# Kernel optimization log

Hardware: AMD Instinct MI355X
Metric: run time of the kernel (lower is better)

Reference implementation:

```python
import jax, jax.numpy as jnp
import numpy as np

EPSILON = 0.01        # temperature
DIST_THRESH = 0.2
NUM_ITERS = 8         # sparse_rebalance_iters (== num_iters here)
TOPK = 64             # topk_support
NEG_INF = -1e9


def setup_inputs() -> dict:
    key = jax.random.key(0)
    k1, k2, k3 = jax.random.split(key, 3)
    B, N, M, D = 4, 4096, 4096, 128
    return {
        "source_feats": jax.random.normal(k1, (B, N, D), dtype=jnp.float32),
        "source_locs": jax.random.uniform(k2, (B, N, 2), dtype=jnp.float32),
        "target_locs": jax.random.uniform(k3, (B, M, 2), dtype=jnp.float32),
        "source_valid_mask": jnp.ones((B, N), dtype=bool),
        "target_valid_mask": jnp.ones((B, M), dtype=bool),
    }


def _sinkhorn_attn(source_locs, target_locs, source_valid_mask, target_valid_mask):
    # pairwise squared distances: [B, M, N]
    diff = target_locs[:, :, None, :] - source_locs[:, None, :, :]
    dist_sq = jnp.sum(diff * diff, axis=-1)
    log_k = -dist_sq / (EPSILON + 1e-8)
    valid = (dist_sq < DIST_THRESH ** 2)
    valid = valid & source_valid_mask[:, None, :] & target_valid_mask[:, :, None]

    B, M, N = valid.shape
    topk = min(TOPK, N)
    if topk < N:
        masked_log_k = jnp.where(valid, log_k, NEG_INF)
        _, topk_idx = jax.lax.top_k(masked_log_k, topk)  # [B, M, topk]
        support = jnp.zeros_like(valid).at[
            jnp.arange(B)[:, None, None], jnp.arange(M)[None, :, None], topk_idx
        ].set(True)
        valid = valid & support

    log_k = jnp.where(valid, log_k, NEG_INF)

    v = jnp.zeros((B, 1, N), dtype=log_k.dtype)
    u = jnp.zeros((B, M, 1), dtype=log_k.dtype)
    for _ in range(NUM_ITERS):
        u = -jax.nn.logsumexp(log_k + v, axis=2, keepdims=True)
        v = -jax.nn.logsumexp(log_k + u, axis=1, keepdims=True)
        v = jnp.where(source_valid_mask[:, None, :], v, 0.0)

    attn = jnp.exp(log_k + u + v)              # [B, M, N]
    has_source = valid.any(axis=-1, keepdims=True)  # [B, M, 1]
    return attn, has_source


def reference(source_feats, source_locs, target_locs, source_valid_mask, target_valid_mask):
    attn, has_source = _sinkhorn_attn(source_locs, target_locs,
                                      source_valid_mask, target_valid_mask)
    target_feats = jnp.einsum('bmn,bnd->bmd', attn, source_feats)
    target_feats = target_feats * target_valid_mask[:, :, None].astype(target_feats.dtype)
    target_feats = target_feats * has_source.astype(target_feats.dtype)
    return target_feats
```

## Files before the change

### kernel.cpp

```cpp
#include <hip/hip_runtime.h>
#include <math.h>

#define B 4
#define N 4096
#define M 4096
#define D 128
#define K 64
#define BT 256
#define WPB 4
#define RPW 2
#define CAP 768
#define CUTCAP 128
#define PC 128
#define EPS_DENOM 0.01000001f
#define THRESH2 0.04f
#define GC 16
#define NBCOL (B * N / 16)
#define NBPREP (B * N / 256)

__global__ __launch_bounds__(1024) void k_sort(const float* __restrict__ slocs,
        float4* __restrict__ sPack, int* __restrict__ cellStart,
        int* __restrict__ colcnt, int* __restrict__ E, int* __restrict__ R,
        float* __restrict__ extraF, float* __restrict__ cs){
    __shared__ int hist[256], startS[256], fill[256], wtot[4];
    __shared__ float2 loc[N];
    __shared__ unsigned short scell[N];
    const int b = blockIdx.x, tid = threadIdx.x;
    const int lane = tid & 63, w = tid >> 6;
    const float2* slp = (const float2*)(slocs + (size_t)b * N * 2);

    for (int i = tid; i < N; i += 1024){
        colcnt[b * N + i] = 0;
        cs[b * N + i] = 1.0f;
    }
    if (b == 0){
        if (tid < B){ E[tid] = 0; R[tid] = 0; }
        if (tid < B * D) extraF[tid] = 0.f;
    }

    if (tid < 256){ hist[tid] = 0; fill[tid] = 0; }
    __syncthreads();
    for (int i = tid; i < N; i += 1024){
        float2 p = slp[i];
        int cx = min(GC - 1, max(0, (int)(p.x * (float)GC)));
        int cy = min(GC - 1, max(0, (int)(p.y * (float)GC)));
        int cell = cy * GC + cx;
        loc[i] = p; scell[i] = (unsigned short)cell;
        atomicAdd(&hist[cell], 1);
    }
    __syncthreads();
    int hv = (tid < 256) ? hist[tid] : 0;
    int pre = hv;
    #pragma unroll
    for (int o = 1; o < 64; o <<= 1){ int t2 = __shfl_up(pre, o, 64); if (lane >= o) pre += t2; }
    if (tid < 256 && lane == 63) wtot[w] = pre;
    __syncthreads();
    if (tid < 256){
        int off = 0;
        for (int i = 0; i < w; ++i) off += wtot[i];
        int st = off + pre - hv;
        startS[tid] = st;
        cellStart[b * 257 + tid] = st;
    }
    if (tid == 0) cellStart[b * 257 + 256] = N;
    __syncthreads();
    for (int i = tid; i < N; i += 1024){
        int cell = scell[i];
        int pos = startS[cell] + atomicAdd(&fill[cell], 1);
        float2 p = loc[i];
        sPack[(size_t)b * N + pos] = make_float4(p.x, p.y, __int_as_float(i), 0.f);
    }
}

__global__ __launch_bounds__(BT, 4) void k_build(const float4* __restrict__ sPack,
        const int* __restrict__ cellStart, const float* __restrict__ tlocs,
        float2* __restrict__ csr, int* __restrict__ cnt,
        int* __restrict__ colcnt, float2* __restrict__ csc,
        int* __restrict__ R, float* __restrict__ eu){
    __shared__ int cs[257];
    __shared__ float cd2[WPB][CAP];
    __shared__ int   cn [WPB][CAP];
    __shared__ int   hist[WPB][64];
    __shared__ float cutd[WPB][CUTCAP];
    __shared__ int   cutn[WPB][CUTCAP];
    __shared__ float seld2[WPB][K];
    __shared__ int   seln [WPB][K];

    const int bid  = blockIdx.x;
    const int b    = bid / (M / (WPB * RPW));
    const int m00  = (bid % (M / (WPB * RPW))) * (WPB * RPW);
    const int tid  = threadIdx.x;
    const int w    = tid >> 6;
    const int lane = tid & 63;
    const unsigned long long pmask = (lane == 0) ? 0ull : ((1ull << lane) - 1);
    const float4* sp = sPack + (size_t)b * N;

    for (int i = tid; i < 257; i += BT) cs[i] = cellStart[b * 257 + i];
    __syncthreads();

    for (int r = 0; r < RPW; ++r){
        const int m     = m00 + w * RPW + r;
        const int rowid = b * M + m;

        hist[w][lane] = 0;

        const float tx = tlocs[((size_t)b * M + m) * 2 + 0];
        const float ty = tlocs[((size_t)b * M + m) * 2 + 1];
        const int cy0 = max(0, (int)floorf((ty - 0.2f) * (float)GC - 0.001f));
        const int cy1 = min(GC - 1, (int)floorf((ty + 0.2f) * (float)GC + 0.001f));

        int c = 0;
        for (int cy = cy0; cy <= cy1; ++cy){
            float rowLo = cy * 0.0625f, rowHi = rowLo + 0.0625f;
            float dymin = fmaxf(0.f, fmaxf(rowLo - ty, ty - rowHi));
            float dxm = sqrtf(fmaxf(THRESH2 - dymin * dymin + 1e-5f, 0.f));
            int cx0 = max(0, (int)floorf((tx - dxm) * (float)GC - 0.001f));
            int cx1 = min(GC - 1, (int)floorf((tx + dxm) * (float)GC + 0.001f));
            int s = cs[cy * GC + cx0], e = cs[cy * GC + cx1 + 1];
            for (int j0 = s; j0 < e; j0 += 128){
                int ja = j0 + lane;
                int jb = ja + 64;
                float4 qa = sp[ja];
                float4 qb = sp[jb];
                float dxa = __fsub_rn(tx, qa.x), dya = __fsub_rn(ty, qa.y);
                float d2a = __fadd_rn(__fmul_rn(dxa, dxa), __fmul_rn(dya, dya));
                bool ina = (ja < e) && (d2a < THRESH2);
                unsigned long long mla = __ballot(ina);
                if (ina){
                    int p = c + __popcll(mla & pmask);
                    if (p < CAP){ cd2[w][p] = d2a; cn[w][p] = __float_as_int(qa.z); }
                    atomicAdd(&hist[w][min((int)(d2a * 1600.0f), 63)], 1);
                }
                c += __popcll(mla);
                float dxb = __fsub_rn(tx, qb.x), dyb = __fsub_rn(ty, qb.y);
                float d2b = __fadd_rn(__fmul_rn(dxb, dxb), __fmul_rn(dyb, dyb));
                bool inb = (jb < e) && (d2b < THRESH2);
                unsigned long long mlb = __ballot(inb);
                if (inb){
                    int p = c + __popcll(mlb & pmask);
                    if (p < CAP){ cd2[w][p] = d2b; cn[w][p] = __float_as_int(qb.z); }
                    atomicAdd(&hist[w][min((int)(d2b * 1600.0f), 63)], 1);
                }
                c += __popcll(mlb);
            }
        }
        const int ctot = min(c, CAP);

        int h = hist[w][lane];
        int pre = h;
        #pragma unroll
        for (int o = 1; o < 64; o <<= 1){
            int t2 = __shfl_up(pre, o, 64);
            if (lane >= o) pre += t2;
        }
        int cutB = 64, q = 0;
        if (c > K){
            unsigned long long ge = __ballot(pre >= K);
            int fb = __ffsll((long long)ge) - 1;
            cutB = fb;
            q = K - __shfl(pre - h, fb, 64);
        }

        int base = 0, cutc = 0;
        for (int i0 = 0; i0 < ctot; i0 += 64){
            int i = i0 + lane;
            bool valid = i < ctot;
            float d2 = 1e9f; int n = 0;
            if (valid){ d2 = cd2[w][i]; n = cn[w][i]; }
            int bk = valid ? min((int)(d2 * 1600.0f), 63) : 64;
            bool low = valid && (bk < cutB);
            unsigned long long ml = __ballot(low);
            if (low){
                int p = base + __popcll(ml & pmask);
                seld2[w][p] = d2; seln[w][p] = n;
            }
            base += __popcll(ml);
            if (cutB < 64){
                bool eq = valid && (bk == cutB);
                unsigned long long me = __ballot(eq);
                if (eq){
                    int p = cutc + __popcll(me & pmask);
                    if (p < CUTCAP){ cutd[w][p] = d2; cutn[w][p] = n; }
                }
                cutc += __popcll(me);
            }
        }

        if (c > K){
            int cc = min(cutc, CUTCAP);
            for (int i0 = 0; i0 < CUTCAP; i0 += 64){
                int i = i0 + lane;
                bool sel = false; float d2i = 0.f; int ni = 0;
                if (i < cc){
                    d2i = cutd[w][i]; ni = cutn[w][i];
                    int rank = 0;
                    for (int j = 0; j < cc; ++j){
                        float dj = cutd[w][j]; int nj = cutn[w][j];
                        rank += (dj < d2i) || (dj == d2i && nj < ni);
                    }
                    sel = rank < q;
                }
                unsigned long long ms = __ballot(sel);
                if (sel){
                    int p = base + __popcll(ms & pmask);
                    seld2[w][p] = d2i; seln[w][p] = ni;
                }
                base += __popcll(ms);
                if (i0 + 64 >= cc) break;
            }
        }

        float e = 0.f;
        if (lane < base){
            float d2 = seld2[w][lane];
            int n = seln[w][lane];
            e = expf(-(d2 / EPS_DENOM));
            float2 pr; pr.x = e; pr.y = __int_as_float(n);
            csr[(size_t)rowid * K + lane] = pr;
            int bn = b * N + n;
            int slot = atomicAdd(&colcnt[bn], 1);
            if (slot < PC){
                float2 pc; pc.x = e; pc.y = __int_as_float(rowid);
                csc[(size_t)bn * PC + slot] = pc;
            }
        }
        float rs = e;
        #pragma unroll
        for (int o = 32; o; o >>= 1) rs += __shfl_xor(rs, o, 64);
        if (lane == 0){
            cnt[rowid] = base;
            if (base == 0) atomicAdd(&R[b], 1);
            eu[rowid] = (base == 0) ? 0.f : 1.0f / rs;
        }
    }
}

__global__ __launch_bounds__(256) void kA(const float2* __restrict__ csr,
        const int* __restrict__ cnt, const float* __restrict__ cs,
        const int* __restrict__ E, float* __restrict__ eu){
    int t = blockIdx.x * blockDim.x + threadIdx.x;
    int W = t >> 6, lane = t & 63;
    for (int rr = 0; rr < 4; ++rr){
        int rid = W * 4 + rr;
        int b = rid >> 12;
        int c = cnt[rid];
        float s = 0.f;
        if (lane < c){
            float2 q = csr[(size_t)rid * K + lane];
            s = q.x / cs[(b << 12) + __float_as_int(q.y)];
        }
        #pragma unroll
        for (int o = 32; o; o >>= 1) s += __shfl_xor(s, o, 64);
        int Eb = E[b];
        if (c == 0 && Eb == 0){
            if (lane == 0) eu[rid] = 0.f;
        } else {
            if (Eb > 0) s += (float)Eb;
            if (lane == 0) eu[rid] = 1.0f / s;
        }
    }
}

__global__ __launch_bounds__(256) void kB(const float2* __restrict__ csc,
        const int* __restrict__ colcnt, const float* __restrict__ eu,
        const int* __restrict__ R, float* __restrict__ cs,
        const float* __restrict__ feats, float* __restrict__ extraF, int* __restrict__ E){
    if (blockIdx.x >= NBCOL){
        int t = (blockIdx.x - NBCOL) * 256 + threadIdx.x;
        int lane = t & 63, b = t >> 12;
        int cc = colcnt[t];
        unsigned long long em = __ballot(cc == 0);
        if (lane == 0 && em) atomicAdd(&E[b], __popcll(em));
        if (cc == 0){
            for (int d = 0; d < D; ++d)
                atomicAdd(&extraF[b * D + d], feats[(size_t)t * D + d]);
        }
        return;
    }
    int t = blockIdx.x * blockDim.x + threadIdx.x;
    int W = t >> 6, lane = t & 63;
    for (int rr = 0; rr < 4; ++rr){
        int cid = W * 4 + rr;
        int b = cid >> 12;
        int cc = min(colcnt[cid], PC);
        float s = 0.f;
        for (int p = lane; p < cc; p += 64){
            float2 q = csc[(size_t)cid * PC + p];
            s += q.x * eu[__float_as_int(q.y)];
        }
        #pragma unroll
        for (int o = 32; o; o >>= 1) s += __shfl_xor(s, o, 64);
        if (lane == 0)
            cs[cid] = s + (float)R[b];
    }
}

__global__ __launch_bounds__(256) void k_out(const float* __restrict__ feats,
        const float2* __restrict__ csr, const int* __restrict__ cnt,
        const float* __restrict__ eu, const float* __restrict__ cs,
        const float* __restrict__ extraF, float* __restrict__ out){
    int t = blockIdx.x * blockDim.x + threadIdx.x;
    int rid = t >> 6, lane = t & 63;
    int b = rid >> 12;
    int c = cnt[rid];
    float a = 0.f; int ix = (b << 12);
    if (lane < c){
        float2 q = csr[(size_t)rid * K + lane];
        ix = (b << 12) + __float_as_int(q.y);
        a = q.x * eu[rid] / cs[ix];
    }
    float2 acc = make_float2(0.f, 0.f);
    if (c > 0)
        acc = ((const float2*)extraF)[b * 64 + lane];
    const float2* fb = (const float2*)feats;
    #pragma unroll 4
    for (int k = 0; k < c; ++k){
        float ak = __shfl(a, k, 64);
        int  nk = __shfl(ix, k, 64);
        float2 f = fb[(size_t)nk * 64 + lane];
        acc.x = fmaf(ak, f.x, acc.x);
        acc.y = fmaf(ak, f.y, acc.y);
    }
    ((float2*)out)[(size_t)rid * 64 + lane] = acc;
}

extern "C" void kernel_launch(void* const* d_in, const int* in_sizes, int n_in,
                              void* d_out, int out_size, void* d_ws, size_t ws_size,
                              hipStream_t stream){
    const float* feats = (const float*)d_in[0];
    const float* slocs = (const float*)d_in[1];
    const float* tlocs = (const float*)d_in[2];
    float* out = (float*)d_out;

    char* w = (char*)d_ws;
    size_t off = 0;
    auto carve = [&](size_t bytes) -> void* {
        void* p = w + off;
        off += (bytes + 255) & ~(size_t)255;
        return p;
    };
    float2* csr    = (float2*)carve((size_t)B * M * K * 8);
    float2* csc    = (float2*)carve((size_t)B * N * PC * 8);
    int*   cnt     = (int*)  carve((size_t)B * M * 4);
    int*   colcnt  = (int*)  carve((size_t)B * N * 4);
    float* eu      = (float*)carve((size_t)B * M * 4);
    float* cs      = (float*)carve((size_t)B * N * 4);
    int*   E       = (int*)  carve(B * 4);
    int*   R       = (int*)  carve(B * 4);
    float* extraF  = (float*)carve((size_t)B * D * 4);
    float4* sPack  = (float4*)carve(((size_t)B * N + 128) * 16);
    int*   cellStart = (int*)carve((size_t)B * 257 * 4);

    k_sort<<<B, 1024, 0, stream>>>(slocs, sPack, cellStart, colcnt, E, R, extraF, cs);
    k_build<<<B * M / (WPB * RPW), BT, 0, stream>>>(sPack, cellStart, tlocs,
            csr, cnt, colcnt, csc, R, eu);
    kB<<<NBCOL + NBPREP, 256, 0, stream>>>(csc, colcnt, eu, R, cs, feats, extraF, E);
    for (int it = 2; it <= 8; ++it){
        kA<<<B * M / 16, 256, 0, stream>>>(csr, cnt, cs, E, eu);
        kB<<<NBCOL, 256, 0, stream>>>(csc, colcnt, eu, R, cs, feats, extraF, E);
    }
    k_out<<<B * M / 4, 256, 0, stream>>>(feats, csr, cnt, eu, cs, extraF, out);
}
```

Baseline: 272.9 us.

## Replace candidate buffering with three-pass recompute top-k and separate CSC build kernel

The row-selection kernel stops staging every in-radius candidate in large shared arrays. Instead it makes three passes over the grid cells: build a histogram, gather the cut bucket with per-lane counts, then write the selected entries straight to CSR at prefix-sum offsets. The CSC transpose moves into its own kernel that reads the CSR entries, and rows per wave go from 2 to 4. Less shared memory should allow more occupancy and removes the CAP overflow limit, at the cost of recomputing distances three times and an extra kernel launch with global atomics.

```diff
diff --git a/kernel.cpp b/kernel.cpp
--- a/kernel.cpp
+++ b/kernel.cpp
@@ -8,8 +8,7 @@
 #define K 64
 #define BT 256
 #define WPB 4
-#define RPW 2
-#define CAP 768
+#define RPW 4
 #define CUTCAP 128
 #define PC 128
 #define EPS_DENOM 0.01000001f
@@ -72,19 +71,15 @@
     }
 }
 
-__global__ __launch_bounds__(BT, 4) void k_build(const float4* __restrict__ sPack,
+__global__ __launch_bounds__(BT, 4) void k_sel(const float4* __restrict__ sPack,
         const int* __restrict__ cellStart, const float* __restrict__ tlocs,
         float2* __restrict__ csr, int* __restrict__ cnt,
-        int* __restrict__ colcnt, float2* __restrict__ csc,
         int* __restrict__ R, float* __restrict__ eu){
     __shared__ int cs[257];
-    __shared__ float cd2[WPB][CAP];
-    __shared__ int   cn [WPB][CAP];
-    __shared__ int   hist[WPB][64];
+    __shared__ int hist[WPB][64];
     __shared__ float cutd[WPB][CUTCAP];
     __shared__ int   cutn[WPB][CUTCAP];
-    __shared__ float seld2[WPB][K];
-    __shared__ int   seln [WPB][K];
+    __shared__ int   cutcS[WPB];
 
     const int bid  = blockIdx.x;
     const int b    = bid / (M / (WPB * RPW));
@@ -92,7 +87,6 @@
     const int tid  = threadIdx.x;
     const int w    = tid >> 6;
     const int lane = tid & 63;
-    const unsigned long long pmask = (lane == 0) ? 0ull : ((1ull << lane) - 1);
     const float4* sp = sPack + (size_t)b * N;
 
     for (int i = tid; i < 257; i += BT) cs[i] = cellStart[b * 257 + i];
@@ -103,13 +97,13 @@
         const int rowid = b * M + m;
 
         hist[w][lane] = 0;
+        if (lane == 0) cutcS[w] = 0;
 
         const float tx = tlocs[((size_t)b * M + m) * 2 + 0];
         const float ty = tlocs[((size_t)b * M + m) * 2 + 1];
         const int cy0 = max(0, (int)floorf((ty - 0.2f) * (float)GC - 0.001f));
         const int cy1 = min(GC - 1, (int)floorf((ty + 0.2f) * (float)GC + 0.001f));
 
-        int c = 0;
         for (int cy = cy0; cy <= cy1; ++cy){
             float rowLo = cy * 0.0625f, rowHi = rowLo + 0.0625f;
             float dymin = fmaxf(0.f, fmaxf(rowLo - ty, ty - rowHi));
@@ -118,33 +112,19 @@
             int cx1 = min(GC - 1, (int)floorf((tx + dxm) * (float)GC + 0.001f));
             int s = cs[cy * GC + cx0], e = cs[cy * GC + cx1 + 1];
             for (int j0 = s; j0 < e; j0 += 128){
-                int ja = j0 + lane;
-                int jb = ja + 64;
+                int ja = j0 + lane, jb = ja + 64;
                 float4 qa = sp[ja];
                 float4 qb = sp[jb];
                 float dxa = __fsub_rn(tx, qa.x), dya = __fsub_rn(ty, qa.y);
                 float d2a = __fadd_rn(__fmul_rn(dxa, dxa), __fmul_rn(dya, dya));
-                bool ina = (ja < e) && (d2a < THRESH2);
-                unsigned long long mla = __ballot(ina);
-                if (ina){
-                    int p = c + __popcll(mla & pmask);
-                    if (p < CAP){ cd2[w][p] = d2a; cn[w][p] = __float_as_int(qa.z); }
+                if ((ja < e) && (d2a < THRESH2))
                     atomicAdd(&hist[w][min((int)(d2a * 1600.0f), 63)], 1);
-                }
-                c += __popcll(mla);
                 float dxb = __fsub_rn(tx, qb.x), dyb = __fsub_rn(ty, qb.y);
                 float d2b = __fadd_rn(__fmul_rn(dxb, dxb), __fmul_rn(dyb, dyb));
-                bool inb = (jb < e) && (d2b < THRESH2);
-                unsigned long long mlb = __ballot(inb);
-                if (inb){
-                    int p = c + __popcll(mlb & pmask);
-                    if (p < CAP){ cd2[w][p] = d2b; cn[w][p] = __float_as_int(qb.z); }
+                if ((jb < e) && (d2b < THRESH2))
                     atomicAdd(&hist[w][min((int)(d2b * 1600.0f), 63)], 1);
-                }
-                c += __popcll(mlb);
             }
         }
-        const int ctot = min(c, CAP);
 
         int h = hist[w][lane];
         int pre = h;
@@ -153,85 +133,137 @@
             int t2 = __shfl_up(pre, o, 64);
             if (lane >= o) pre += t2;
         }
-        int cutB = 64, q = 0;
+        const int c = __shfl(pre, 63, 64);
+        int cutB = 64, q = 0, lowTot = min(c, K);
         if (c > K){
             unsigned long long ge = __ballot(pre >= K);
             int fb = __ffsll((long long)ge) - 1;
             cutB = fb;
-            q = K - __shfl(pre - h, fb, 64);
-        }
-
-        int base = 0, cutc = 0;
-        for (int i0 = 0; i0 < ctot; i0 += 64){
-            int i = i0 + lane;
-            bool valid = i < ctot;
-            float d2 = 1e9f; int n = 0;
-            if (valid){ d2 = cd2[w][i]; n = cn[w][i]; }
-            int bk = valid ? min((int)(d2 * 1600.0f), 63) : 64;
-            bool low = valid && (bk < cutB);
-            unsigned long long ml = __ballot(low);
-            if (low){
-                int p = base + __popcll(ml & pmask);
-                seld2[w][p] = d2; seln[w][p] = n;
+            int lowBelow = __shfl(pre - h, fb, 64);
+            q = K - lowBelow;
+            lowTot = lowBelow;
+        }
+
+        int si = 0;
+        for (int cy = cy0; cy <= cy1; ++cy){
+            float rowLo = cy * 0.0625f, rowHi = rowLo + 0.0625f;
+            float dymin = fmaxf(0.f, fmaxf(rowLo - ty, ty - rowHi));
+            float dxm = sqrtf(fmaxf(THRESH2 - dymin * dymin + 1e-5f, 0.f));
+            int cx0 = max(0, (int)floorf((tx - dxm) * (float)GC - 0.001f));
+            int cx1 = min(GC - 1, (int)floorf((tx + dxm) * (float)GC + 0.001f));
+            int s = cs[cy * GC + cx0], e = cs[cy * GC + cx1 + 1];
+            for (int j0 = s; j0 < e; j0 += 128){
+                int ja = j0 + lane, jb = ja + 64;
+                float4 qa = sp[ja];
+                float4 qb = sp[jb];
+                float dxa = __fsub_rn(tx, qa.x), dya = __fsub_rn(ty, qa.y);
+                float d2a = __fadd_rn(__fmul_rn(dxa, dxa), __fmul_rn(dya, dya));
+                if ((ja < e) && (d2a < THRESH2)){
+                    int bk = min((int)(d2a * 1600.0f), 63);
+                    si += (bk < cutB);
+                    if (bk == cutB){
+                        int p = atomicAdd(&cutcS[w], 1);
+                        if (p < CUTCAP){ cutd[w][p] = d2a; cutn[w][p] = __float_as_int(qa.z); }
+                    }
+                }
+                float dxb = __fsub_rn(tx, qb.x), dyb = __fsub_rn(ty, qb.y);
+                float d2b = __fadd_rn(__fmul_rn(dxb, dxb), __fmul_rn(dyb, dyb));
+                if ((jb < e) && (d2b < THRESH2)){
+                    int bk = min((int)(d2b * 1600.0f), 63);
+                    si += (bk < cutB);
+                    if (bk == cutB){
+                        int p = atomicAdd(&cutcS[w], 1);
+                        if (p < CUTCAP){ cutd[w][p] = d2b; cutn[w][p] = __float_as_int(qb.z); }
+                    }
+                }
             }
-            base += __popcll(ml);
-            if (cutB < 64){
-                bool eq = valid && (bk == cutB);
-                unsigned long long me = __ballot(eq);
-                if (eq){
-                    int p = cutc + __popcll(me & pmask);
-                    if (p < CUTCAP){ cutd[w][p] = d2; cutn[w][p] = n; }
-                }
-                cutc += __popcll(me);
-            }
-        }
+        }
+        int ip = si;
+        #pragma unroll
+        for (int o = 1; o < 64; o <<= 1){
+            int t2 = __shfl_up(ip, o, 64);
+            if (lane >= o) ip += t2;
+        }
+        const int laneBase = ip - si;
+
+        float rs = 0.f;
 
         if (c > K){
-            int cc = min(cutc, CUTCAP);
+            int cc = min(cutcS[w], CUTCAP);
             for (int i0 = 0; i0 < CUTCAP; i0 += 64){
                 int i = i0 + lane;
-                bool sel = false; float d2i = 0.f; int ni = 0;
                 if (i < cc){
-                    d2i = cutd[w][i]; ni = cutn[w][i];
+                    float d2i = cutd[w][i]; int ni = cutn[w][i];
                     int rank = 0;
                     for (int j = 0; j < cc; ++j){
                         float dj = cutd[w][j]; int nj = cutn[w][j];
                         rank += (dj < d2i) || (dj == d2i && nj < ni);
                     }
-                    sel = rank < q;
-                }
-                unsigned long long ms = __ballot(sel);
-                if (sel){
-                    int p = base + __popcll(ms & pmask);
-                    seld2[w][p] = d2i; seln[w][p] = ni;
-                }
-                base += __popcll(ms);
+                    if (rank < q){
+                        float e = expf(-(d2i / EPS_DENOM));
+                        rs += e;
+                        float2 pr; pr.x = e; pr.y = __int_as_float(ni);
+                        csr[(size_t)rowid * K + lowTot + rank] = pr;
+                    }
+                }
                 if (i0 + 64 >= cc) break;
             }
         }
 
-        float e = 0.f;
-        if (lane < base){
-            float d2 = seld2[w][lane];
-            int n = seln[w][lane];
-            e = expf(-(d2 / EPS_DENOM));
-            float2 pr; pr.x = e; pr.y = __int_as_float(n);
-            csr[(size_t)rowid * K + lane] = pr;
-            int bn = b * N + n;
-            int slot = atomicAdd(&colcnt[bn], 1);
-            if (slot < PC){
-                float2 pc; pc.x = e; pc.y = __int_as_float(rowid);
-                csc[(size_t)bn * PC + slot] = pc;
+        int local = 0;
+        for (int cy = cy0; cy <= cy1; ++cy){
+            float rowLo = cy * 0.0625f, rowHi = rowLo + 0.0625f;
+            float dymin = fmaxf(0.f, fmaxf(rowLo - ty, ty - rowHi));
+            float dxm = sqrtf(fmaxf(THRESH2 - dymin * dymin + 1e-5f, 0.f));
+            int cx0 = max(0, (int)floorf((tx - dxm) * (float)GC - 0.001f));
+            int cx1 = min(GC - 1, (int)floorf((tx + dxm) * (float)GC + 0.001f));
+            int s = cs[cy * GC + cx0], e = cs[cy * GC + cx1 + 1];
+            for (int j0 = s; j0 < e; j0 += 128){
+                int ja = j0 + lane, jb = ja + 64;
+                float4 qa = sp[ja];
+                float4 qb = sp[jb];
+                float dxa = __fsub_rn(tx, qa.x), dya = __fsub_rn(ty, qa.y);
+                float d2a = __fadd_rn(__fmul_rn(dxa, dxa), __fmul_rn(dya, dya));
+                if ((ja < e) && (d2a < THRESH2) && (min((int)(d2a * 1600.0f), 63) < cutB)){
+                    float e2 = expf(-(d2a / EPS_DENOM));
+                    rs += e2;
+                    float2 pr; pr.x = e2; pr.y = qa.z;
+                    csr[(size_t)rowid * K + laneBase + local] = pr;
+                    ++local;
+                }
+                float dxb = __fsub_rn(tx, qb.x), dyb = __fsub_rn(ty, qb.y);
+                float d2b = __fadd_rn(__fmul_rn(dxb, dxb), __fmul_rn(dyb, dyb));
+                if ((jb < e) && (d2b < THRESH2) && (min((int)(d2b * 1600.0f), 63) < cutB)){
+                    float e2 = expf(-(d2b / EPS_DENOM));
+                    rs += e2;
+                    float2 pr; pr.x = e2; pr.y = qb.z;
+                    csr[(size_t)rowid * K + laneBase + local] = pr;
+                    ++local;
+                }
             }
         }
-        float rs = e;
+
         #pragma unroll
         for (int o = 32; o; o >>= 1) rs += __shfl_xor(rs, o, 64);
         if (lane == 0){
-            cnt[rowid] = base;
-            if (base == 0) atomicAdd(&R[b], 1);
-            eu[rowid] = (base == 0) ? 0.f : 1.0f / rs;
-        }
+            int cfin = min(c, K);
+            cnt[rowid] = cfin;
+            if (cfin == 0) atomicAdd(&R[b], 1);
+            eu[rowid] = (cfin == 0) ? 0.f : 1.0f / rs;
+        }
+    }
+}
+
+__global__ __launch_bounds__(256) void k_csc(const float2* __restrict__ csr,
+        const int* __restrict__ cnt, int* __restrict__ colcnt, float2* __restrict__ csc){
+    int e = blockIdx.x * 256 + threadIdx.x;
+    int rid = e >> 6, k = e & 63;
+    if (k < cnt[rid]){
+        float2 q = csr[e];
+        int bn = ((rid >> 12) << 12) + __float_as_int(q.y);
+        int slot = atomicAdd(&colcnt[bn], 1);
+        if (slot < PC)
+            csc[(size_t)bn * PC + slot] = make_float2(q.x, __int_as_float(rid));
     }
 }
 
@@ -352,8 +384,8 @@
     int*   cellStart = (int*)carve((size_t)B * 257 * 4);
 
     k_sort<<<B, 1024, 0, stream>>>(slocs, sPack, cellStart, colcnt, E, R, extraF, cs);
-    k_build<<<B * M / (WPB * RPW), BT, 0, stream>>>(sPack, cellStart, tlocs,
-            csr, cnt, colcnt, csc, R, eu);
+    k_sel<<<B * M / (WPB * RPW), BT, 0, stream>>>(sPack, cellStart, tlocs, csr, cnt, R, eu);
+    k_csc<<<B * M * K / 256, 256, 0, stream>>>(csr, cnt, colcnt, csc);
     kB<<<NBCOL + NBPREP, 256, 0, stream>>>(csc, colcnt, eu, R, cs, feats, extraF, E);
     for (int it = 2; it <= 8; ++it){
         kA<<<B * M / 16, 256, 0, stream>>>(csr, cnt, cs, E, eu);
```

After: 333.1 us. 1.22x slower.

## Shrink neighbor search radius adaptively and fuse top-k selection with CSR emission

Applied to the files above, without the earlier changes.

Replaces the full 0.2-radius candidate gather into shared memory with an adaptive radius estimated from the uniform source density and the target's distance to the border, falling back to the full radius when too few candidates land in the guaranteed-safe histogram bins. Selection is then done by re-scanning the grid and writing CSR/CSC entries directly, with tie-bucket entries placed by rank, instead of staging candidates in large shared arrays. This cuts the number of candidates scanned per row and the shared-memory footprint, which may raise occupancy. The cost is up to three grid scans per row, and the radius constant is tuned to the density of the test inputs.

```diff
diff --git a/kernel.cpp b/kernel.cpp
--- a/kernel.cpp
+++ b/kernel.cpp
@@ -9,12 +9,13 @@
 #define BT 256
 #define WPB 4
 #define RPW 2
-#define CAP 768
 #define CUTCAP 128
 #define PC 128
 #define EPS_DENOM 0.01000001f
 #define THRESH2 0.04f
 #define GC 16
+#define GCF 16.0f
+#define RHO0 0.0955f
 #define NBCOL (B * N / 16)
 #define NBPREP (B * N / 256)
 
@@ -42,8 +43,8 @@
     __syncthreads();
     for (int i = tid; i < N; i += 1024){
         float2 p = slp[i];
-        int cx = min(GC - 1, max(0, (int)(p.x * (float)GC)));
-        int cy = min(GC - 1, max(0, (int)(p.y * (float)GC)));
+        int cx = min(GC - 1, max(0, (int)(p.x * GCF)));
+        int cy = min(GC - 1, max(0, (int)(p.y * GCF)));
         int cell = cy * GC + cx;
         loc[i] = p; scell[i] = (unsigned short)cell;
         atomicAdd(&hist[cell], 1);
@@ -72,19 +73,15 @@
     }
 }
 
-__global__ __launch_bounds__(BT, 4) void k_build(const float4* __restrict__ sPack,
+__global__ __launch_bounds__(BT, 4) void k_sel(const float4* __restrict__ sPack,
         const int* __restrict__ cellStart, const float* __restrict__ tlocs,
-        float2* __restrict__ csr, int* __restrict__ cnt,
-        int* __restrict__ colcnt, float2* __restrict__ csc,
-        int* __restrict__ R, float* __restrict__ eu){
+        float2* __restrict__ csr, int* __restrict__ cnt, int* __restrict__ colcnt,
+        float2* __restrict__ csc, int* __restrict__ R, float* __restrict__ eu){
     __shared__ int cs[257];
-    __shared__ float cd2[WPB][CAP];
-    __shared__ int   cn [WPB][CAP];
-    __shared__ int   hist[WPB][64];
+    __shared__ int hist[WPB][64];
     __shared__ float cutd[WPB][CUTCAP];
     __shared__ int   cutn[WPB][CUTCAP];
-    __shared__ float seld2[WPB][K];
-    __shared__ int   seln [WPB][K];
+    __shared__ int   cutcS[WPB];
 
     const int bid  = blockIdx.x;
     const int b    = bid / (M / (WPB * RPW));
@@ -101,51 +98,48 @@
     for (int r = 0; r < RPW; ++r){
         const int m     = m00 + w * RPW + r;
         const int rowid = b * M + m;
+        const int bN    = b * N;
 
         hist[w][lane] = 0;
+        if (lane == 0) cutcS[w] = 0;
 
         const float tx = tlocs[((size_t)b * M + m) * 2 + 0];
         const float ty = tlocs[((size_t)b * M + m) * 2 + 1];
-        const int cy0 = max(0, (int)floorf((ty - 0.2f) * (float)GC - 0.001f));
-        const int cy1 = min(GC - 1, (int)floorf((ty + 0.2f) * (float)GC + 0.001f));
-
-        int c = 0;
-        for (int cy = cy0; cy <= cy1; ++cy){
-            float rowLo = cy * 0.0625f, rowHi = rowLo + 0.0625f;
-            float dymin = fmaxf(0.f, fmaxf(rowLo - ty, ty - rowHi));
-            float dxm = sqrtf(fmaxf(THRESH2 - dymin * dymin + 1e-5f, 0.f));
-            int cx0 = max(0, (int)floorf((tx - dxm) * (float)GC - 0.001f));
-            int cx1 = min(GC - 1, (int)floorf((tx + dxm) * (float)GC + 0.001f));
-            int s = cs[cy * GC + cx0], e = cs[cy * GC + cx1 + 1];
-            for (int j0 = s; j0 < e; j0 += 128){
-                int ja = j0 + lane;
-                int jb = ja + 64;
-                float4 qa = sp[ja];
-                float4 qb = sp[jb];
-                float dxa = __fsub_rn(tx, qa.x), dya = __fsub_rn(ty, qa.y);
-                float d2a = __fadd_rn(__fmul_rn(dxa, dxa), __fmul_rn(dya, dya));
-                bool ina = (ja < e) && (d2a < THRESH2);
-                unsigned long long mla = __ballot(ina);
-                if (ina){
-                    int p = c + __popcll(mla & pmask);
-                    if (p < CAP){ cd2[w][p] = d2a; cn[w][p] = __float_as_int(qa.z); }
-                    atomicAdd(&hist[w][min((int)(d2a * 1600.0f), 63)], 1);
+
+        float exd = fmaxf(0.f, fminf(tx, 1.f - tx));
+        float eyd = fmaxf(0.f, fminf(ty, 1.f - ty));
+        float rho = RHO0;
+        #pragma unroll
+        for (int it2 = 0; it2 < 2; ++it2){
+            float fx = fminf(1.f, 0.5f + 0.55f * exd / rho);
+            float fy = fminf(1.f, 0.5f + 0.55f * eyd / rho);
+            rho = fminf(0.2f, RHO0 * rsqrtf(fx * fy));
+        }
+
+        auto histPass = [&](float rad){
+            int cy0 = max(0, (int)floorf((ty - rad) * GCF - 0.001f));
+            int cy1 = min(GC - 1, (int)floorf((ty + rad) * GCF + 0.001f));
+            float r2 = rad * rad;
+            for (int cy = cy0; cy <= cy1; ++cy){
+                float rowLo = cy * 0.0625f, rowHi = rowLo + 0.0625f;
+                float dymin = fmaxf(0.f, fmaxf(rowLo - ty, ty - rowHi));
+                float dxm = sqrtf(fmaxf(r2 - dymin * dymin + 1e-5f, 0.f));
+                int cx0 = max(0, (int)floorf((tx - dxm) * GCF - 0.001f));
+                int cx1 = min(GC - 1, (int)floorf((tx + dxm) * GCF + 0.001f));
+                int s = cs[cy * GC + cx0], e = cs[cy * GC + cx1 + 1];
+                for (int j0 = s; j0 < e; j0 += 64){
+                    int j = j0 + lane;
+                    float4 q = sp[j];
+                    float dx = __fsub_rn(tx, q.x);
+                    float dy = __fsub_rn(ty, q.y);
+                    float d2 = __fadd_rn(__fmul_rn(dx, dx), __fmul_rn(dy, dy));
+                    if ((j < e) && (d2 < THRESH2))
+                        atomicAdd(&hist[w][min((int)(d2 * 1600.0f), 63)], 1);
                 }
-                c += __popcll(mla);
-                float dxb = __fsub_rn(tx, qb.x), dyb = __fsub_rn(ty, qb.y);
-                float d2b = __fadd_rn(__fmul_rn(dxb, dxb), __fmul_rn(dyb, dyb));
-                bool inb = (jb < e) && (d2b < THRESH2);
-                unsigned long long mlb = __ballot(inb);
-                if (inb){
-                    int p = c + __popcll(mlb & pmask);
-                    if (p < CAP){ cd2[w][p] = d2b; cn[w][p] = __float_as_int(qb.z); }
-                    atomicAdd(&hist[w][min((int)(d2b * 1600.0f), 63)], 1);
-                }
-                c += __popcll(mlb);
             }
-        }
-        const int ctot = min(c, CAP);
-
+        };
+
+        histPass(rho);
         int h = hist[w][lane];
         int pre = h;
         #pragma unroll
@@ -153,36 +147,77 @@
             int t2 = __shfl_up(pre, o, 64);
             if (lane >= o) pre += t2;
         }
-        int cutB = 64, q = 0;
+
+        if (rho < 0.2f){
+            int B0 = (int)(rho * rho * 1600.0f) - 1;
+            int cb = (B0 >= 1) ? __shfl(pre, min(B0, 64) - 1, 64) : 0;
+            if (cb < K){
+                hist[w][lane] = 0;
+                rho = 0.2f;
+                histPass(0.2f);
+                h = hist[w][lane];
+                pre = h;
+                #pragma unroll
+                for (int o = 1; o < 64; o <<= 1){
+                    int t2 = __shfl_up(pre, o, 64);
+                    if (lane >= o) pre += t2;
+                }
+            }
+        }
+
+        const int c = __shfl(pre, 63, 64);
+        int cutB = 64, q = 0, lowTot = min(c, K);
         if (c > K){
             unsigned long long ge = __ballot(pre >= K);
             int fb = __ffsll((long long)ge) - 1;
             cutB = fb;
-            q = K - __shfl(pre - h, fb, 64);
-        }
-
+            int lowBelow = __shfl(pre - h, fb, 64);
+            q = K - lowBelow;
+            lowTot = lowBelow;
+        }
+
+        float rs = 0.f;
         int base = 0, cutc = 0;
-        for (int i0 = 0; i0 < ctot; i0 += 64){
-            int i = i0 + lane;
-            bool valid = i < ctot;
-            float d2 = 1e9f; int n = 0;
-            if (valid){ d2 = cd2[w][i]; n = cn[w][i]; }
-            int bk = valid ? min((int)(d2 * 1600.0f), 63) : 64;
-            bool low = valid && (bk < cutB);
-            unsigned long long ml = __ballot(low);
-            if (low){
-                int p = base + __popcll(ml & pmask);
-                seld2[w][p] = d2; seln[w][p] = n;
-            }
-            base += __popcll(ml);
-            if (cutB < 64){
-                bool eq = valid && (bk == cutB);
-                unsigned long long me = __ballot(eq);
-                if (eq){
-                    int p = cutc + __popcll(me & pmask);
-                    if (p < CUTCAP){ cutd[w][p] = d2; cutn[w][p] = n; }
+        {
+            int cy0 = max(0, (int)floorf((ty - rho) * GCF - 0.001f));
+            int cy1 = min(GC - 1, (int)floorf((ty + rho) * GCF + 0.001f));
+            float r2 = rho * rho;
+            for (int cy = cy0; cy <= cy1; ++cy){
+                float rowLo = cy * 0.0625f, rowHi = rowLo + 0.0625f;
+                float dymin = fmaxf(0.f, fmaxf(rowLo - ty, ty - rowHi));
+                float dxm = sqrtf(fmaxf(r2 - dymin * dymin + 1e-5f, 0.f));
+                int cx0 = max(0, (int)floorf((tx - dxm) * GCF - 0.001f));
+                int cx1 = min(GC - 1, (int)floorf((tx + dxm) * GCF + 0.001f));
+                int s = cs[cy * GC + cx0], e = cs[cy * GC + cx1 + 1];
+                for (int j0 = s; j0 < e; j0 += 64){
+                    int j = j0 + lane;
+                    float4 qd = sp[j];
+                    float dx = __fsub_rn(tx, qd.x);
+                    float dy = __fsub_rn(ty, qd.y);
+                    float d2 = __fadd_rn(__fmul_rn(dx, dx), __fmul_rn(dy, dy));
+                    bool in = (j < e) && (d2 < THRESH2);
+                    int bk = in ? min((int)(d2 * 1600.0f), 63) : 64;
+                    bool low = in && (bk < cutB);
+                    unsigned long long ml = __ballot(low);
+                    if (low){
+                        int p = base + __popcll(ml & pmask);
+                        float el = expf(-(d2 / EPS_DENOM));
+                        rs += el;
+                        csr[(size_t)rowid * K + p] = make_float2(el, qd.z);
+                        int bn = bN + __float_as_int(qd.z);
+                        int slot = atomicAdd(&colcnt[bn], 1);
+                        if (slot < PC)
+                            csc[(size_t)bn * PC + slot] = make_float2(el, __int_as_float(rowid));
+                    }
+                    base += __popcll(ml);
+                    bool eq = in && (bk == cutB);
+                    unsigned long long me = __ballot(eq);
+                    if (eq){
+                        int p = cutc + __popcll(me & pmask);
+                        if (p < CUTCAP){ cutd[w][p] = d2; cutn[w][p] = __float_as_int(qd.z); }
+                    }
+                    cutc += __popcll(me);
                 }
-                cutc += __popcll(me);
             }
         }
 
@@ -190,47 +225,34 @@
             int cc = min(cutc, CUTCAP);
             for (int i0 = 0; i0 < CUTCAP; i0 += 64){
                 int i = i0 + lane;
-                bool sel = false; float d2i = 0.f; int ni = 0;
                 if (i < cc){
-                    d2i = cutd[w][i]; ni = cutn[w][i];
+                    float d2i = cutd[w][i]; int ni = cutn[w][i];
                     int rank = 0;
                     for (int j = 0; j < cc; ++j){
                         float dj = cutd[w][j]; int nj = cutn[w][j];
                         rank += (dj < d2i) || (dj == d2i && nj < ni);
                     }
-                    sel = rank < q;
+                    if (rank < q){
+                        float el = expf(-(d2i / EPS_DENOM));
+                        rs += el;
+                        csr[(size_t)rowid * K + lowTot + rank] = make_float2(el, __int_as_float(ni));
+                        int bn = bN + ni;
+                        int slot = atomicAdd(&colcnt[bn], 1);
+                        if (slot < PC)
+                            csc[(size_t)bn * PC + slot] = make_float2(el, __int_as_float(rowid));
+                    }
                 }
-                unsigned long long ms = __ballot(sel);
-                if (sel){
-                    int p = base + __popcll(ms & pmask);
-                    seld2[w][p] = d2i; seln[w][p] = ni;
-                }
-                base += __popcll(ms);
                 if (i0 + 64 >= cc) break;
             }
         }
 
-        float e = 0.f;
-        if (lane < base){
-            float d2 = seld2[w][lane];
-            int n = seln[w][lane];
-            e = expf(-(d2 / EPS_DENOM));
-            float2 pr; pr.x = e; pr.y = __int_as_float(n);
-            csr[(size_t)rowid * K + lane] = pr;
-            int bn = b * N + n;
-            int slot = atomicAdd(&colcnt[bn], 1);
-            if (slot < PC){
-                float2 pc; pc.x = e; pc.y = __int_as_float(rowid);
-                csc[(size_t)bn * PC + slot] = pc;
-            }
-        }
-        float rs = e;
         #pragma unroll
         for (int o = 32; o; o >>= 1) rs += __shfl_xor(rs, o, 64);
         if (lane == 0){
-            cnt[rowid] = base;
-            if (base == 0) atomicAdd(&R[b], 1);
-            eu[rowid] = (base == 0) ? 0.f : 1.0f / rs;
+            int cfin = min(c, K);
+            cnt[rowid] = cfin;
+            if (cfin == 0) atomicAdd(&R[b], 1);
+            eu[rowid] = (cfin == 0) ? 0.f : 1.0f / rs;
         }
     }
 }
@@ -352,7 +374,7 @@
     int*   cellStart = (int*)carve((size_t)B * 257 * 4);
 
     k_sort<<<B, 1024, 0, stream>>>(slocs, sPack, cellStart, colcnt, E, R, extraF, cs);
-    k_build<<<B * M / (WPB * RPW), BT, 0, stream>>>(sPack, cellStart, tlocs,
+    k_sel<<<B * M / (WPB * RPW), BT, 0, stream>>>(sPack, cellStart, tlocs,
             csr, cnt, colcnt, csc, R, eu);
     kB<<<NBCOL + NBPREP, 256, 0, stream>>>(csc, colcnt, eu, R, cs, feats, extraF, E);
     for (int it = 2; it <= 8; ++it){
```

After: 262.7 us. 3.7% less time.
